# Kernel optimization log

Measured on AMD Instinct MI355X. Metric: run time of the kernel, lower is better.

The kernel has to match this reference:

```python
import jax, jax.numpy as jnp
import numpy as np

B = 16          # number of trees (batch)
H = 256         # hidden_size == feature_size
S = 16          # Tree.num_sem
C = 5           # max_child_num (complete C-ary tree)
L = 6           # tree depth: leaves at level L, internal levels 0..L-1
N_LEAF = C**L                     # 15625
N_INT = (C**L - 1) // (C - 1)     # 3906 internal nodes, level-l offset = (C^l-1)/(C-1)


def setup_inputs() -> dict:
    key = jax.random.key(0)
    ks = jax.random.split(key, 20)
    rn = lambda k, shp, s=0.05: jax.random.normal(k, shp, dtype=jnp.float32) * s
    return {
        "leaf_box": jax.random.normal(ks[0], (B, N_LEAF, 4), dtype=jnp.float32),
        "leaf_sem": jax.random.uniform(ks[1], (B, N_LEAF, S), dtype=jnp.float32),
        "internal_box": jax.random.normal(ks[2], (B, N_INT, 4), dtype=jnp.float32),
        "node_type": jax.random.randint(ks[3], (B, N_INT), 0, 3, dtype=jnp.int32),
        "eps": jax.random.normal(ks[4], (B, H), dtype=jnp.float32),
        "W_box": rn(ks[5], (4, H)), "b_box": jnp.zeros((H,), jnp.float32),
        "W_sem": rn(ks[6], (S, H)), "b_sem": jnp.zeros((H,), jnp.float32),
        "W_node": rn(ks[7], (3, C * H, H)), "b_node": jnp.zeros((3, H), jnp.float32),
        "W1": rn(ks[8], (H, H)), "b1": jnp.zeros((H,), jnp.float32),
        "Wmu": rn(ks[9], (H, H)), "bmu": jnp.zeros((H,), jnp.float32),
        "Wvar": rn(ks[10], (H, H)), "bvar": jnp.zeros((H,), jnp.float32),
    }


def reference(leaf_box, leaf_sem, internal_box, node_type, eps,
              W_box, b_box, W_sem, b_sem, W_node, b_node,
              W1, b1, Wmu, bmu, Wvar, bvar):
    box_enc = lambda b: jax.nn.relu(b @ W_box + b_box)
    # LeafEncoder: relu-box-encoding + relu-sem-encoding
    feats = box_enc(leaf_box) + jax.nn.relu(leaf_sem @ W_sem + b_sem)  # [B, N_LEAF, H]
    # Bottom-up over internal levels (static loop over L=6 levels)
    for l in range(L - 1, -1, -1):
        n = C ** l
        off = (C ** l - 1) // (C - 1)
        child = feats.reshape(B, n, C * H)  # children flattened per parent (child_exists==1)
        # Apply all 3 branch encoders (vertical/horizontal/stack), select by node label
        y_all = jnp.einsum('bnk,tkh->bnth', child, W_node) + b_node          # [B,n,3,H]
        sel = jax.nn.one_hot(node_type[:, off:off + n], 3, dtype=child.dtype)  # [B,n,3]
        y = jnp.einsum('bnth,bnt->bnh', y_all, sel)
        feats = jax.nn.relu(y) + box_enc(internal_box[:, off:off + n])
    root = feats[:, 0]  # [B, H]
    # Sampler (variational, probabilistic)
    enc = jax.nn.relu(root @ W1 + b1)
    mu = enc @ Wmu + bmu
    logvar = enc @ Wvar + bvar
    std = jnp.exp(0.5 * logvar)
    kld = 1.0 + logvar - mu ** 2 - jnp.exp(logvar)
    return jnp.concatenate([eps * std + mu, kld], axis=1)  # [B, 2H]
```

## Files before the change

kernel.cpp:

```cpp
#include <hip/hip_runtime.h>


#define B_ 16
#define H_ 256
#define NLEAF 15625
#define NINT 3906

typedef __bf16 bf16_t;
typedef bf16_t bf16x8 __attribute__((ext_vector_type(8)));
typedef bf16_t bf16x4 __attribute__((ext_vector_type(4)));
typedef float f32x4 __attribute__((ext_vector_type(4)));

__device__ __forceinline__ void gl2lds16(const bf16_t* g, bf16_t* l) {
  __builtin_amdgcn_global_load_lds((const __attribute__((address_space(1))) void*)g,
                                   (__attribute__((address_space(3))) void*)l,
                                   16, 0, 0);
}

__global__ __launch_bounds__(256) void prep_kernel(const float* __restrict__ W_node,
                                                   bf16_t* __restrict__ Wt,
                                                   int* __restrict__ counters) {
  if (blockIdx.x == 0 && threadIdx.x < 18) counters[threadIdx.x] = 0;
  const int t = blockIdx.x / 80;
  const int kc = blockIdx.x % 80;
  const int h = threadIdx.x;
  const float* srcp = W_node + (size_t)t * 1280 * 256 + h;
  bf16_t* dstp = Wt + ((size_t)(t * 256 + h)) * 1280;
#pragma unroll
  for (int k0 = kc * 16; k0 < kc * 16 + 16; k0 += 8) {
    bf16x8 v;
#pragma unroll
    for (int j = 0; j < 8; ++j) v[j] = (bf16_t)srcp[(size_t)(k0 + j) * 256];
    *(bf16x8*)(dstp + k0) = v;
  }
}

__global__ __launch_bounds__(256) void leaf_kernel(
    const float* __restrict__ leaf_box, const float* __restrict__ leaf_sem,
    const float* __restrict__ W_box, const float* __restrict__ b_box,
    const float* __restrict__ W_sem, const float* __restrict__ b_sem,
    bf16_t* __restrict__ f6) {
  const int lane = threadIdx.x & 63;
  const int wave = threadIdx.x >> 6;
  const int h0 = lane * 4;
  float wb[4][4], ws[16][4], bb[4], bs[4];
#pragma unroll
  for (int j = 0; j < 4; ++j) {
    float4 v = *(const float4*)(W_box + j * H_ + h0);
    wb[j][0] = v.x; wb[j][1] = v.y; wb[j][2] = v.z; wb[j][3] = v.w;
  }
#pragma unroll
  for (int j = 0; j < 16; ++j) {
    float4 v = *(const float4*)(W_sem + j * H_ + h0);
    ws[j][0] = v.x; ws[j][1] = v.y; ws[j][2] = v.z; ws[j][3] = v.w;
  }
  {
    float4 v = *(const float4*)(b_box + h0);
    bb[0] = v.x; bb[1] = v.y; bb[2] = v.z; bb[3] = v.w;
    float4 u = *(const float4*)(b_sem + h0);
    bs[0] = u.x; bs[1] = u.y; bs[2] = u.z; bs[3] = u.w;
  }
  const int ROWS = B_ * NLEAF;
  const int stride = gridDim.x * 4;
  for (int row = blockIdx.x * 4 + wave; row < ROWS; row += stride) {
    float4 bx = *(const float4*)(leaf_box + (size_t)row * 4);
    const float4* sp = (const float4*)(leaf_sem + (size_t)row * 16);
    float4 sv0 = sp[0], sv1 = sp[1], sv2 = sp[2], sv3 = sp[3];
    bf16x4 o;
#pragma unroll
    for (int c = 0; c < 4; ++c) {
      float s1 = fmaf(wb[0][c], bx.x, fmaf(wb[1][c], bx.y,
                 fmaf(wb[2][c], bx.z, fmaf(wb[3][c], bx.w, bb[c]))));
      float s2 = bs[c];
      s2 = fmaf(ws[0][c], sv0.x, s2);  s2 = fmaf(ws[1][c], sv0.y, s2);
      s2 = fmaf(ws[2][c], sv0.z, s2);  s2 = fmaf(ws[3][c], sv0.w, s2);
      s2 = fmaf(ws[4][c], sv1.x, s2);  s2 = fmaf(ws[5][c], sv1.y, s2);
      s2 = fmaf(ws[6][c], sv1.z, s2);  s2 = fmaf(ws[7][c], sv1.w, s2);
      s2 = fmaf(ws[8][c], sv2.x, s2);  s2 = fmaf(ws[9][c], sv2.y, s2);
      s2 = fmaf(ws[10][c], sv2.z, s2); s2 = fmaf(ws[11][c], sv2.w, s2);
      s2 = fmaf(ws[12][c], sv3.x, s2); s2 = fmaf(ws[13][c], sv3.y, s2);
      s2 = fmaf(ws[14][c], sv3.z, s2); s2 = fmaf(ws[15][c], sv3.w, s2);
      o[c] = (bf16_t)(fmaxf(s1, 0.f) + fmaxf(s2, 0.f));
    }
    *(bf16x4*)(f6 + (size_t)row * H_ + h0) = o;
  }
}

__global__ __launch_bounds__(256) void bucket_kernel(const int* __restrict__ node_type,
                                                     int* __restrict__ counters,
                                                     int2* __restrict__ buckets) {
  __shared__ int lcnt[18];
  __shared__ int lbase[18];
  const int tid = threadIdx.x;
  if (tid < 18) lcnt[tid] = 0;
  __syncthreads();

  int idx = blockIdx.x * 256 + tid;
  bool active = idx < B_ * NINT;
  int t = 0, key = 0, mypos = 0;
  int2 e;
  int base = 0, nl_cap = 0;
  if (active) {
    int b = idx / NINT;
    int j = idx - b * NINT;
    int l, off;
    if (j >= 781)      { l = 5; off = 781; }
    else if (j >= 156) { l = 4; off = 156; }
    else if (j >= 31)  { l = 3; off = 31; }
    else if (j >= 6)   { l = 2; off = 6; }
    else if (j >= 1)   { l = 1; off = 1; }
    else               { l = 0; off = 0; }
    const int n_tab[6]    = {1, 5, 25, 125, 625, 3125};
    const int nn_tab[6]   = {5, 25, 125, 625, 3125, 15625};
    const int base_tab[6] = {0, 48, 288, 1488, 7488, 37488};
    int n_l = n_tab[l], nn = nn_tab[l];
    t = node_type[idx];
    int i = j - off;
    e.x = b * n_l + i;
    e.y = b * nn + 5 * i;
    base = base_tab[l];
    nl_cap = B_ * n_l;
    key = l * 3 + t;
    mypos = atomicAdd(&lcnt[key], 1);
  }
  __syncthreads();
  if (tid < 18) {
    int c = lcnt[tid];
    lbase[tid] = c ? atomicAdd(&counters[tid], c) : 0;
  }
  __syncthreads();
  if (active) {
    buckets[base + t * nl_cap + lbase[key] + mypos] = e;
  }
}

__global__ __launch_bounds__(256) void level_kernel(
    const bf16_t* __restrict__ src, bf16_t* __restrict__ dst,
    const int2* __restrict__ bucket, const int* __restrict__ counters,
    const bf16_t* __restrict__ Wt, const float* __restrict__ b_node,
    const float* __restrict__ ibox, const float* __restrict__ W_box,
    const float* __restrict__ b_box, int n_l, int off_l, int cap) {
  const int t = blockIdx.y;
  const int cnt = counters[t];
  const int tile0 = blockIdx.x * 128;
  if (tile0 >= cnt) return;
  const int nblk = blockIdx.z;
  const int2* rd = bucket + (size_t)t * cap;

  __shared__ __align__(16) bf16_t Asm[2][128][64];
  __shared__ __align__(16) bf16_t Bsm[2][128][64];

  const int tid = threadIdx.x;
  const int lane = tid & 63;
  const int wave = tid >> 6;
  const int wm = wave & 1, wn = wave >> 1;
  const int quad = lane >> 4;
  const int l15 = lane & 15;

  const int r8 = tid >> 3;
  const int sc = tid & 7;
  const bf16_t* wsrc = Wt + ((size_t)t * 256 + nblk * 128) * 1280;
  const bf16_t* aptr[4];
  const bf16_t* bptr[4];
#pragma unroll
  for (int i = 0; i < 4; ++i) {
    int r = i * 32 + r8;
    int gch = sc ^ ((r >> 1) & 7);
    int ai = tile0 + r;
    if (ai >= cnt) ai = cnt - 1;
    aptr[i] = src + (size_t)rd[ai].y * H_ + gch * 8;
    bptr[i] = wsrc + (size_t)r * 1280 + gch * 8;
  }

  f32x4 acc[4][4];
#pragma unroll
  for (int i = 0; i < 4; ++i)
#pragma unroll
    for (int j = 0; j < 4; ++j) acc[i][j] = (f32x4){0.f, 0.f, 0.f, 0.f};

  const int sw = (l15 >> 1) & 7;
  const int pc0 = ((0 * 4 + quad) ^ sw) * 8;
  const int pc1 = ((1 * 4 + quad) ^ sw) * 8;

#define STAGE(buf, ks)                                          \
  {                                                             \
    const int ko = (ks) * 64;                                   \
    bf16_t* la = &Asm[buf][0][0] + wave * 512;                  \
    bf16_t* lb = &Bsm[buf][0][0] + wave * 512;                  \
    _Pragma("unroll") for (int i = 0; i < 4; ++i)               \
        gl2lds16(aptr[i] + ko, la + i * 2048);                  \
    _Pragma("unroll") for (int i = 0; i < 4; ++i)               \
        gl2lds16(bptr[i] + ko, lb + i * 2048);                  \
  }

  STAGE(0, 0)
  for (int ks = 0; ks < 20; ++ks) {
    const int buf = ks & 1;
    __syncthreads();
    bf16x8 af0[4], af1[4], bf0[4], bf1[4];
#pragma unroll
    for (int am = 0; am < 4; ++am) {
      af0[am] = *(const bf16x8*)(&Asm[buf][wm * 64 + am * 16 + l15][pc0]);
      af1[am] = *(const bf16x8*)(&Asm[buf][wm * 64 + am * 16 + l15][pc1]);
    }
#pragma unroll
    for (int bn = 0; bn < 4; ++bn) {
      bf0[bn] = *(const bf16x8*)(&Bsm[buf][wn * 64 + bn * 16 + l15][pc0]);
      bf1[bn] = *(const bf16x8*)(&Bsm[buf][wn * 64 + bn * 16 + l15][pc1]);
    }
    if (ks + 1 < 20) STAGE(buf ^ 1, ks + 1)
#pragma unroll
    for (int am = 0; am < 4; ++am)
#pragma unroll
      for (int bn = 0; bn < 4; ++bn)
        acc[am][bn] = __builtin_amdgcn_mfma_f32_16x16x32_bf16(af0[am], bf0[bn], acc[am][bn], 0, 0, 0);
#pragma unroll
    for (int am = 0; am < 4; ++am)
#pragma unroll
      for (int bn = 0; bn < 4; ++bn)
        acc[am][bn] = __builtin_amdgcn_mfma_f32_16x16x32_bf16(af1[am], bf1[bn], acc[am][bn], 0, 0, 0);
  }
#undef STAGE

  float wbv[4][6];
#pragma unroll
  for (int bn = 0; bn < 4; ++bn) {
    int col = nblk * 128 + wn * 64 + bn * 16 + l15;
    wbv[bn][0] = W_box[col];
    wbv[bn][1] = W_box[H_ + col];
    wbv[bn][2] = W_box[2 * H_ + col];
    wbv[bn][3] = W_box[3 * H_ + col];
    wbv[bn][4] = b_box[col];
    wbv[bn][5] = b_node[t * H_ + col];
  }
#pragma unroll
  for (int am = 0; am < 4; ++am) {
    int orow[4]; float4 bxv[4]; bool valid[4];
#pragma unroll
    for (int r = 0; r < 4; ++r) {
      int gidx = tile0 + wm * 64 + am * 16 + quad * 4 + r;
      valid[r] = (gidx < cnt);
      int ic = valid[r] ? gidx : (cnt - 1);
      int orw = rd[ic].x;
      orow[r] = orw;
      int b = orw / n_l;
      int i = orw - b * n_l;
      bxv[r] = *(const float4*)(ibox + ((size_t)b * NINT + off_l + i) * 4);
    }
#pragma unroll
    for (int bn = 0; bn < 4; ++bn) {
      int col = nblk * 128 + wn * 64 + bn * 16 + l15;
#pragma unroll
      for (int r = 0; r < 4; ++r) {
        if (!valid[r]) continue;
        float y = fmaxf(acc[am][bn][r] + wbv[bn][5], 0.f);
        float be = fmaf(wbv[bn][0], bxv[r].x,
                   fmaf(wbv[bn][1], bxv[r].y,
                   fmaf(wbv[bn][2], bxv[r].z,
                   fmaf(wbv[bn][3], bxv[r].w, wbv[bn][4]))));
        be = fmaxf(be, 0.f);
        dst[(size_t)orow[r] * H_ + col] = (bf16_t)(y + be);
      }
    }
  }
}

__global__ __launch_bounds__(256) void head_kernel(
    const bf16_t* __restrict__ f0, const float* __restrict__ eps,
    const float* __restrict__ W1, const float* __restrict__ b1,
    const float* __restrict__ Wmu, const float* __restrict__ bmu,
    const float* __restrict__ Wvar, const float* __restrict__ bvar,
    float* __restrict__ out) {
  __shared__ float root[256];
  __shared__ float enc[256];
  int b = blockIdx.x, h = threadIdx.x;
  root[h] = (float)f0[b * H_ + h];
  __syncthreads();
  float a = b1[h];
  for (int k = 0; k < 256; ++k) a = fmaf(root[k], W1[k * H_ + h], a);
  enc[h] = fmaxf(a, 0.f);
  __syncthreads();
  float m = bmu[h], lv = bvar[h];
  for (int k = 0; k < 256; ++k) {
    float e = enc[k];
    m = fmaf(e, Wmu[k * H_ + h], m);
    lv = fmaf(e, Wvar[k * H_ + h], lv);
  }
  float stdv = expf(0.5f * lv);
  float kld = 1.f + lv - m * m - expf(lv);
  out[b * 512 + h] = eps[b * H_ + h] * stdv + m;
  out[b * 512 + 256 + h] = kld;
}

extern "C" void kernel_launch(void* const* d_in, const int* in_sizes, int n_in,
                              void* d_out, int out_size, void* d_ws, size_t ws_size,
                              hipStream_t stream) {
  const float* leaf_box     = (const float*)d_in[0];
  const float* leaf_sem     = (const float*)d_in[1];
  const float* internal_box = (const float*)d_in[2];
  const int*   node_type    = (const int*)d_in[3];
  const float* eps          = (const float*)d_in[4];
  const float* W_box        = (const float*)d_in[5];
  const float* b_box        = (const float*)d_in[6];
  const float* W_sem        = (const float*)d_in[7];
  const float* b_sem        = (const float*)d_in[8];
  const float* W_node       = (const float*)d_in[9];
  const float* b_node       = (const float*)d_in[10];
  const float* W1           = (const float*)d_in[11];
  const float* b1           = (const float*)d_in[12];
  const float* Wmu          = (const float*)d_in[13];
  const float* bmu          = (const float*)d_in[14];
  const float* Wvar         = (const float*)d_in[15];
  const float* bvar         = (const float*)d_in[16];
  float* out = (float*)d_out;

  char* p = (char*)d_ws;
  auto alloc = [&](size_t bytes) {
    char* r = p;
    p += (bytes + 255) & ~(size_t)255;
    return r;
  };
  bf16_t* Wt = (bf16_t*)alloc((size_t)3 * 256 * 1280 * 2);
  const int n_tab[7] = {1, 5, 25, 125, 625, 3125, 15625};
  bf16_t* f[7];
  for (int l = 0; l <= 6; ++l) f[l] = (bf16_t*)alloc((size_t)B_ * n_tab[l] * H_ * 2);
  int* counters = (int*)alloc(18 * 4);
  int2* buckets = (int2*)alloc((size_t)187488 * 8);

  hipLaunchKernelGGL(prep_kernel, dim3(240), dim3(256), 0, stream, W_node, Wt, counters);
  hipLaunchKernelGGL(leaf_kernel, dim3(2048), dim3(256), 0, stream,
                     leaf_box, leaf_sem, W_box, b_box, W_sem, b_sem, f[6]);
  hipLaunchKernelGGL(bucket_kernel, dim3((B_ * NINT + 255) / 256), dim3(256), 0, stream,
                     node_type, counters, buckets);

  const int lvl_base[6] = {0, 48, 288, 1488, 7488, 37488};
  const int off_tab[6]  = {0, 1, 6, 31, 156, 781};
  for (int l = 5; l >= 0; --l) {
    int cap = B_ * n_tab[l];
    int tiles = (cap + 127) / 128;
    hipLaunchKernelGGL(level_kernel, dim3(tiles, 3, 2), dim3(256), 0, stream,
                       f[l + 1], f[l], buckets + lvl_base[l], counters + l * 3,
                       Wt, b_node, internal_box, W_box, b_box,
                       n_tab[l], off_tab[l], cap);
  }
  hipLaunchKernelGGL(head_kernel, dim3(16), dim3(256), 0, stream,
                     f[0], eps, W1, b1, Wmu, bmu, Wvar, bvar, out);
}
```

Measured before the change: 401.2 us.

## Use MFMA for leaf encoding and triple-buffer level GEMM with narrower K-steps

```diff
diff --git a/kernel.cpp b/kernel.cpp
--- a/kernel.cpp
+++ b/kernel.cpp
@@ -42,47 +42,68 @@
     bf16_t* __restrict__ f6) {
   const int lane = threadIdx.x & 63;
   const int wave = threadIdx.x >> 6;
-  const int h0 = lane * 4;
-  float wb[4][4], ws[16][4], bb[4], bs[4];
-#pragma unroll
-  for (int j = 0; j < 4; ++j) {
-    float4 v = *(const float4*)(W_box + j * H_ + h0);
-    wb[j][0] = v.x; wb[j][1] = v.y; wb[j][2] = v.z; wb[j][3] = v.w;
-  }
-#pragma unroll
-  for (int j = 0; j < 16; ++j) {
-    float4 v = *(const float4*)(W_sem + j * H_ + h0);
-    ws[j][0] = v.x; ws[j][1] = v.y; ws[j][2] = v.z; ws[j][3] = v.w;
-  }
-  {
-    float4 v = *(const float4*)(b_box + h0);
-    bb[0] = v.x; bb[1] = v.y; bb[2] = v.z; bb[3] = v.w;
-    float4 u = *(const float4*)(b_sem + h0);
-    bs[0] = u.x; bs[1] = u.y; bs[2] = u.z; bs[3] = u.w;
-  }
-  const int ROWS = B_ * NLEAF;
-  const int stride = gridDim.x * 4;
-  for (int row = blockIdx.x * 4 + wave; row < ROWS; row += stride) {
-    float4 bx = *(const float4*)(leaf_box + (size_t)row * 4);
-    const float4* sp = (const float4*)(leaf_sem + (size_t)row * 16);
-    float4 sv0 = sp[0], sv1 = sp[1], sv2 = sp[2], sv3 = sp[3];
-    bf16x4 o;
-#pragma unroll
-    for (int c = 0; c < 4; ++c) {
-      float s1 = fmaf(wb[0][c], bx.x, fmaf(wb[1][c], bx.y,
-                 fmaf(wb[2][c], bx.z, fmaf(wb[3][c], bx.w, bb[c]))));
-      float s2 = bs[c];
-      s2 = fmaf(ws[0][c], sv0.x, s2);  s2 = fmaf(ws[1][c], sv0.y, s2);
-      s2 = fmaf(ws[2][c], sv0.z, s2);  s2 = fmaf(ws[3][c], sv0.w, s2);
-      s2 = fmaf(ws[4][c], sv1.x, s2);  s2 = fmaf(ws[5][c], sv1.y, s2);
-      s2 = fmaf(ws[6][c], sv1.z, s2);  s2 = fmaf(ws[7][c], sv1.w, s2);
-      s2 = fmaf(ws[8][c], sv2.x, s2);  s2 = fmaf(ws[9][c], sv2.y, s2);
-      s2 = fmaf(ws[10][c], sv2.z, s2); s2 = fmaf(ws[11][c], sv2.w, s2);
-      s2 = fmaf(ws[12][c], sv3.x, s2); s2 = fmaf(ws[13][c], sv3.y, s2);
-      s2 = fmaf(ws[14][c], sv3.z, s2); s2 = fmaf(ws[15][c], sv3.w, s2);
-      o[c] = (bf16_t)(fmaxf(s1, 0.f) + fmaxf(s2, 0.f));
-    }
-    *(bf16x4*)(f6 + (size_t)row * H_ + h0) = o;
+  const int q = lane >> 4;
+  const int c = lane & 15;
+  const int hh = wave & 1;
+  const int gw = wave >> 1;
+
+  bf16x8 wsem[8], wbox[8];
+#pragma unroll
+  for (int T = 0; T < 8; ++T) {
+    const int hb = (hh * 8 + T) * 16 + c;
+    bf16x8 a;
+#pragma unroll
+    for (int j = 0; j < 8; ++j) a[j] = (bf16_t)0.f;
+    if (q < 2) {
+#pragma unroll
+      for (int j = 0; j < 8; ++j) a[j] = (bf16_t)W_sem[(q * 8 + j) * H_ + hb];
+    } else if (q == 2) {
+      a[0] = (bf16_t)b_sem[hb];
+    }
+    wsem[T] = a;
+    bf16x8 b;
+#pragma unroll
+    for (int j = 0; j < 8; ++j) b[j] = (bf16_t)0.f;
+    if (q == 0) {
+#pragma unroll
+      for (int j = 0; j < 4; ++j) b[j] = (bf16_t)W_box[j * H_ + hb];
+      b[4] = (bf16_t)b_box[hb];
+    }
+    wbox[T] = b;
+  }
+
+  const int NG = (B_ * NLEAF) / 16;
+  const int gstride = gridDim.x * 2;
+  for (int g = blockIdx.x * 2 + gw; g < NG; g += gstride) {
+    const int row = g * 16 + c;
+    bf16x8 xs, xb;
+#pragma unroll
+    for (int j = 0; j < 8; ++j) { xs[j] = (bf16_t)0.f; xb[j] = (bf16_t)0.f; }
+    if (q < 2) {
+      const float4* sp = (const float4*)(leaf_sem + (size_t)row * 16 + q * 8);
+      float4 s0 = sp[0], s1 = sp[1];
+      xs[0] = (bf16_t)s0.x; xs[1] = (bf16_t)s0.y; xs[2] = (bf16_t)s0.z; xs[3] = (bf16_t)s0.w;
+      xs[4] = (bf16_t)s1.x; xs[5] = (bf16_t)s1.y; xs[6] = (bf16_t)s1.z; xs[7] = (bf16_t)s1.w;
+    } else if (q == 2) {
+      xs[0] = (bf16_t)1.0f;
+    }
+    if (q == 0) {
+      float4 bx = *(const float4*)(leaf_box + (size_t)row * 4);
+      xb[0] = (bf16_t)bx.x; xb[1] = (bf16_t)bx.y; xb[2] = (bf16_t)bx.z; xb[3] = (bf16_t)bx.w;
+      xb[4] = (bf16_t)1.0f;
+    }
+    bf16_t* orow = f6 + (size_t)row * H_ + hh * 128 + q * 4;
+#pragma unroll
+    for (int T = 0; T < 8; ++T) {
+      f32x4 z = {0.f, 0.f, 0.f, 0.f};
+      f32x4 as = __builtin_amdgcn_mfma_f32_16x16x32_bf16(wsem[T], xs, z, 0, 0, 0);
+      f32x4 ab = __builtin_amdgcn_mfma_f32_16x16x32_bf16(wbox[T], xb, z, 0, 0, 0);
+      bf16x4 o;
+#pragma unroll
+      for (int r = 0; r < 4; ++r)
+        o[r] = (bf16_t)(fmaxf(as[r], 0.f) + fmaxf(ab[r], 0.f));
+      *(bf16x4*)(orow + T * 16) = o;
+    }
   }
 }
 
@@ -147,8 +168,8 @@
   const int nblk = blockIdx.z;
   const int2* rd = bucket + (size_t)t * cap;
 
-  __shared__ __align__(16) bf16_t Asm[2][128][64];
-  __shared__ __align__(16) bf16_t Bsm[2][128][64];
+  __shared__ __align__(16) bf16_t Asm[3][128][32];
+  __shared__ __align__(16) bf16_t Bsm[3][128][32];
 
   const int tid = threadIdx.x;
   const int lane = tid & 63;
@@ -157,19 +178,18 @@
   const int quad = lane >> 4;
   const int l15 = lane & 15;
 
-  const int r8 = tid >> 3;
-  const int sc = tid & 7;
+  const int r4 = lane >> 2;
+  const int c4 = lane & 3;
   const bf16_t* wsrc = Wt + ((size_t)t * 256 + nblk * 128) * 1280;
-  const bf16_t* aptr[4];
-  const bf16_t* bptr[4];
-#pragma unroll
-  for (int i = 0; i < 4; ++i) {
-    int r = i * 32 + r8;
-    int gch = sc ^ ((r >> 1) & 7);
+  const bf16_t* aptr[2];
+  const bf16_t* bptr[2];
+#pragma unroll
+  for (int i = 0; i < 2; ++i) {
+    int r = wave * 32 + i * 16 + r4;
     int ai = tile0 + r;
     if (ai >= cnt) ai = cnt - 1;
-    aptr[i] = src + (size_t)rd[ai].y * H_ + gch * 8;
-    bptr[i] = wsrc + (size_t)r * 1280 + gch * 8;
+    aptr[i] = src + (size_t)rd[ai].y * H_ + c4 * 8;
+    bptr[i] = wsrc + (size_t)r * 1280 + c4 * 8;
   }
 
   f32x4 acc[4][4];
@@ -178,47 +198,39 @@
 #pragma unroll
     for (int j = 0; j < 4; ++j) acc[i][j] = (f32x4){0.f, 0.f, 0.f, 0.f};
 
-  const int sw = (l15 >> 1) & 7;
-  const int pc0 = ((0 * 4 + quad) ^ sw) * 8;
-  const int pc1 = ((1 * 4 + quad) ^ sw) * 8;
-
-#define STAGE(buf, ks)                                          \
-  {                                                             \
-    const int ko = (ks) * 64;                                   \
-    bf16_t* la = &Asm[buf][0][0] + wave * 512;                  \
-    bf16_t* lb = &Bsm[buf][0][0] + wave * 512;                  \
-    _Pragma("unroll") for (int i = 0; i < 4; ++i)               \
-        gl2lds16(aptr[i] + ko, la + i * 2048);                  \
-    _Pragma("unroll") for (int i = 0; i < 4; ++i)               \
-        gl2lds16(bptr[i] + ko, lb + i * 2048);                  \
+#define STAGE(buf, ks)                                  \
+  {                                                     \
+    const int ko = (ks) * 32;                           \
+    bf16_t* la = &Asm[buf][0][0] + wave * 1024;         \
+    bf16_t* lb = &Bsm[buf][0][0] + wave * 1024;         \
+    gl2lds16(aptr[0] + ko, la);                         \
+    gl2lds16(aptr[1] + ko, la + 512);                   \
+    gl2lds16(bptr[0] + ko, lb);                         \
+    gl2lds16(bptr[1] + ko, lb + 512);                   \
   }
 
   STAGE(0, 0)
-  for (int ks = 0; ks < 20; ++ks) {
-    const int buf = ks & 1;
-    __syncthreads();
-    bf16x8 af0[4], af1[4], bf0[4], bf1[4];
-#pragma unroll
-    for (int am = 0; am < 4; ++am) {
-      af0[am] = *(const bf16x8*)(&Asm[buf][wm * 64 + am * 16 + l15][pc0]);
-      af1[am] = *(const bf16x8*)(&Asm[buf][wm * 64 + am * 16 + l15][pc1]);
-    }
-#pragma unroll
-    for (int bn = 0; bn < 4; ++bn) {
-      bf0[bn] = *(const bf16x8*)(&Bsm[buf][wn * 64 + bn * 16 + l15][pc0]);
-      bf1[bn] = *(const bf16x8*)(&Bsm[buf][wn * 64 + bn * 16 + l15][pc1]);
-    }
-    if (ks + 1 < 20) STAGE(buf ^ 1, ks + 1)
+  STAGE(1, 1)
+  int buf = 0, nxb = 2;
+  for (int ks = 0; ks < 40; ++ks) {
+    if (ks < 39) asm volatile("s_waitcnt vmcnt(4)" ::: "memory");
+    else         asm volatile("s_waitcnt vmcnt(0)" ::: "memory");
+    __builtin_amdgcn_s_barrier();
+    bf16x8 af[4], bfr[4];
 #pragma unroll
     for (int am = 0; am < 4; ++am)
+      af[am] = *(const bf16x8*)(&Asm[buf][wm * 64 + am * 16 + l15][quad * 8]);
+#pragma unroll
+    for (int bn = 0; bn < 4; ++bn)
+      bfr[bn] = *(const bf16x8*)(&Bsm[buf][wn * 64 + bn * 16 + l15][quad * 8]);
+    if (ks < 38) STAGE(nxb, ks + 2)
+#pragma unroll
+    for (int am = 0; am < 4; ++am)
 #pragma unroll
       for (int bn = 0; bn < 4; ++bn)
-        acc[am][bn] = __builtin_amdgcn_mfma_f32_16x16x32_bf16(af0[am], bf0[bn], acc[am][bn], 0, 0, 0);
-#pragma unroll
-    for (int am = 0; am < 4; ++am)
-#pragma unroll
-      for (int bn = 0; bn < 4; ++bn)
-        acc[am][bn] = __builtin_amdgcn_mfma_f32_16x16x32_bf16(af1[am], bf1[bn], acc[am][bn], 0, 0, 0);
+        acc[am][bn] = __builtin_amdgcn_mfma_f32_16x16x32_bf16(af[am], bfr[bn], acc[am][bn], 0, 0, 0);
+    buf = (buf == 2) ? 0 : buf + 1;
+    nxb = (nxb == 2) ? 0 : nxb + 1;
   }
 #undef STAGE
 
@@ -328,7 +340,7 @@
   int2* buckets = (int2*)alloc((size_t)187488 * 8);
 
   hipLaunchKernelGGL(prep_kernel, dim3(240), dim3(256), 0, stream, W_node, Wt, counters);
-  hipLaunchKernelGGL(leaf_kernel, dim3(2048), dim3(256), 0, stream,
+  hipLaunchKernelGGL(leaf_kernel, dim3(1024), dim3(256), 0, stream,
                      leaf_box, leaf_sem, W_box, b_box, W_sem, b_sem, f[6]);
   hipLaunchKernelGGL(bucket_kernel, dim3((B_ * NINT + 255) / 256), dim3(256), 0, stream,
                      node_type, counters, buckets);
```

Result: no change. 401.0 us (-0.1%).
